# Performance work log

Hardware: AMD Instinct MI355X
Metric: run time of the kernel (lower is better)

The kernel has to match this reference:

```python
import jax, jax.numpy as jnp
import numpy as np

NEG_INF = -1e9  # matches the TF additive-mask constant


def setup_inputs() -> dict:
    key = jax.random.key(0)
    k1, k2, k3 = jax.random.split(key, 3)
    B, Tq, Tk, D = 8, 2048, 2048, 1024
    decoder_outputs = jax.random.normal(k1, (B, Tq, D), dtype=jnp.float32)
    encoder_outputs = jax.random.normal(k2, (B, Tk, D), dtype=jnp.float32)
    encoder_mask = jax.random.randint(k3, (B, Tk), 0, 2, dtype=jnp.int32)
    return {
        "decoder_outputs": decoder_outputs,
        "encoder_outputs": encoder_outputs,
        "encoder_mask": encoder_mask,
    }


def reference(decoder_outputs, encoder_outputs, encoder_mask):
    # score[b, q, k] = <dec[b, q], enc[b, k]>  (no 1/sqrt(d) scaling in original)
    score = jnp.einsum("bqd,bkd->bqk", decoder_outputs, encoder_outputs)
    m = encoder_mask.astype(score.dtype)[:, None, :]  # [B, 1, Tk]
    score = score + (1.0 - m) * NEG_INF
    attention_weights = jax.nn.softmax(score, axis=-1)
    context_vector = jnp.einsum("bqk,bkd->bqd", attention_weights, encoder_outputs)
    return (context_vector, attention_weights)
```

## Files before the change

### kernel.cpp

```cpp
#include <hip/hip_runtime.h>
#include <cstddef>
#include <cstdint>

typedef _Float16 f16x8 __attribute__((ext_vector_type(8)));
typedef _Float16 f16x4 __attribute__((ext_vector_type(4)));
typedef float f32x4 __attribute__((ext_vector_type(4)));

static constexpr int BATCH = 8;
static constexpr int TQ = 2048;
static constexpr int TK = 2048;
static constexpr int DIM = 1024;
static constexpr size_t CTX_ELEMS = (size_t)BATCH * TQ * DIM;
static constexpr size_t ATT_ELEMS = (size_t)BATCH * TQ * TK;

static constexpr size_t WS_DEC = 0;
static constexpr size_t WS_ENC = WS_DEC + CTX_ELEMS;
static constexpr size_t WS_ENCT = WS_ENC + CTX_ELEMS;
static constexpr size_t WS_W = WS_ENCT + CTX_ELEMS;
static constexpr size_t WS_NEEDED_BYTES = (WS_W + ATT_ELEMS) * 2;

__device__ __forceinline__ void async16(const void* g, const void* l) {
  __builtin_amdgcn_global_load_lds(
      (const __attribute__((address_space(1))) unsigned int*)g,
      (__attribute__((address_space(3))) unsigned int*)l, 16, 0, 0);
}

__device__ __forceinline__ f16x8 cvt8(float4 a, float4 b) {
  f16x8 h;
  h[0] = (_Float16)a.x; h[1] = (_Float16)a.y; h[2] = (_Float16)a.z; h[3] = (_Float16)a.w;
  h[4] = (_Float16)b.x; h[5] = (_Float16)b.y; h[6] = (_Float16)b.z; h[7] = (_Float16)b.w;
  return h;
}


__global__ __launch_bounds__(256) void convert_kernel(
    const float* __restrict__ enc, const float* __restrict__ dec,
    _Float16* __restrict__ enc16, _Float16* __restrict__ encT,
    _Float16* __restrict__ dec16) {
  __shared__ _Float16 sT[64 * 72];
  const int k0 = blockIdx.x * 64, d0 = blockIdx.y * 64, b = blockIdx.z;
  const int t = threadIdx.x;
  const int krow = t >> 2;
  const int dcol = (t & 3) * 16;

  const float* src = enc + ((size_t)b * TK + k0 + krow) * DIM + d0 + dcol;
  float4 f0 = *(const float4*)(src);
  float4 f1 = *(const float4*)(src + 4);
  float4 f2 = *(const float4*)(src + 8);
  float4 f3 = *(const float4*)(src + 12);
  _Float16 h[16];
#pragma unroll
  for (int i = 0; i < 4; i++) {
    h[i]      = (_Float16)((&f0.x)[i]);
    h[i + 4]  = (_Float16)((&f1.x)[i]);
    h[i + 8]  = (_Float16)((&f2.x)[i]);
    h[i + 12] = (_Float16)((&f3.x)[i]);
  }
  _Float16* dsts = enc16 + ((size_t)b * TK + k0 + krow) * DIM + d0 + dcol;
  *(f16x8*)dsts = *(const f16x8*)&h[0];
  *(f16x8*)(dsts + 8) = *(const f16x8*)&h[8];
#pragma unroll
  for (int i = 0; i < 16; i++)
    sT[(dcol + i) * 72 + krow] = h[i];

  {
    const int bid = ((blockIdx.z * gridDim.y) + blockIdx.y) * gridDim.x + blockIdx.x;
    size_t base = (size_t)bid * 4096 + (size_t)t * 16;
    float4 a0 = *(const float4*)(dec + base);
    float4 a1 = *(const float4*)(dec + base + 4);
    float4 a2 = *(const float4*)(dec + base + 8);
    float4 a3 = *(const float4*)(dec + base + 12);
    *(f16x8*)(dec16 + base) = cvt8(a0, a1);
    *(f16x8*)(dec16 + base + 8) = cvt8(a2, a3);
  }

  __syncthreads();

  const int drow = t >> 2;
  const int kg = (t & 3) * 16;
  f16x8 v0 = *(const f16x8*)&sT[drow * 72 + kg];
  f16x8 v1 = *(const f16x8*)&sT[drow * 72 + kg + 8];
  _Float16* dst = encT + ((size_t)b * DIM + d0 + drow) * TK + k0 + kg;
  *(f16x8*)dst = v0;
  *(f16x8*)(dst + 8) = v1;
}

static constexpr int HT = 8192;

template <int KD>
__device__ __forceinline__ void stage_ht(const _Float16* __restrict__ Xb,
                                         _Float16* ht, int khalf, int w, int lane) {
#pragma unroll
  for (int j = 0; j < 2; ++j) {
    const int r = w * 16 + j * 8 + (lane >> 3);
    const int slot = (lane & 7) ^ (r & 7);
    async16(Xb + (size_t)r * KD + khalf + slot * 8, ht + (w * 16 + j * 8) * 64);
  }
}

template <int M, int N, int K>
__global__ __launch_bounds__(512, 2) void gemm_cf(
    const _Float16* __restrict__ A, const _Float16* __restrict__ B,
    float* __restrict__ C) {
  __shared__ _Float16 lds[65536];
  constexpr int T = K / 64;

  const int b = blockIdx.x, nt = blockIdx.y, mt = blockIdx.z;
  const int tid = threadIdx.x;
  const int lane = tid & 63, w = tid >> 6;
  const int tm = lane & 15, quad = lane >> 4;
  const int wr = w >> 2, wc = w & 3;

  const _Float16* Ab = A + ((size_t)b * M + mt * 256) * K;
  const _Float16* Bb = B + ((size_t)b * N + nt * 256) * K;
  const _Float16* src[4] = {Ab, Ab + (size_t)128 * K, Bb, Bb + (size_t)128 * K};

  const int aht = wr;
  const int bht = 2 + (wc >> 1);
  const int brow = (wc & 1) * 64;

  const int s0 = (quad ^ (tm & 7)) * 8;
  const int s1 = s0 ^ 32;

  f32x4 acc[8][4] = {};

#pragma unroll
  for (int q = 0; q < 4; ++q)
    stage_ht<K>(src[q], lds + q * HT, 0, w, lane);
  asm volatile("s_waitcnt vmcnt(0)" ::: "memory");
  __builtin_amdgcn_s_barrier();

  for (int t = 0; t < T; ++t) {
    const int p = t & 1, np = p ^ 1;
    const _Float16* hA = lds + (p * 4 + aht) * HT;
    const _Float16* hB = lds + (p * 4 + bht) * HT;
    f16x8 aF[4], bF[4];

#pragma unroll
    for (int j = 0; j < 4; ++j)
      bF[j] = *(const f16x8*)(hB + (brow + j * 16 + tm) * 64 + s0);
#pragma unroll
    for (int i = 0; i < 4; ++i)
      aF[i] = *(const f16x8*)(hA + (i * 16 + tm) * 64 + s0);
    if (t + 1 < T) {
      const int kh = (t + 1) * 64;
#pragma unroll
      for (int q = 0; q < 4; ++q)
        stage_ht<K>(src[q], lds + (np * 4 + q) * HT, kh, w, lane);
    }
    __builtin_amdgcn_s_barrier();
    __builtin_amdgcn_s_setprio(1);
#pragma unroll
    for (int i = 0; i < 4; ++i)
#pragma unroll
      for (int j = 0; j < 4; ++j)
        acc[i][j] = __builtin_amdgcn_mfma_f32_16x16x32_f16(aF[i], bF[j], acc[i][j], 0, 0, 0);
    __builtin_amdgcn_s_setprio(0);
    __builtin_amdgcn_s_barrier();

#pragma unroll
    for (int i = 0; i < 4; ++i)
      aF[i] = *(const f16x8*)(hA + (64 + i * 16 + tm) * 64 + s0);
    __builtin_amdgcn_s_barrier();
    __builtin_amdgcn_s_setprio(1);
#pragma unroll
    for (int i = 0; i < 4; ++i)
#pragma unroll
      for (int j = 0; j < 4; ++j)
        acc[4 + i][j] = __builtin_amdgcn_mfma_f32_16x16x32_f16(aF[i], bF[j], acc[4 + i][j], 0, 0, 0);
    __builtin_amdgcn_s_setprio(0);
    __builtin_amdgcn_s_barrier();

#pragma unroll
    for (int j = 0; j < 4; ++j)
      bF[j] = *(const f16x8*)(hB + (brow + j * 16 + tm) * 64 + s1);
#pragma unroll
    for (int i = 0; i < 4; ++i)
      aF[i] = *(const f16x8*)(hA + (i * 16 + tm) * 64 + s1);
    __builtin_amdgcn_s_barrier();
    __builtin_amdgcn_s_setprio(1);
#pragma unroll
    for (int i = 0; i < 4; ++i)
#pragma unroll
      for (int j = 0; j < 4; ++j)
        acc[i][j] = __builtin_amdgcn_mfma_f32_16x16x32_f16(aF[i], bF[j], acc[i][j], 0, 0, 0);
    __builtin_amdgcn_s_setprio(0);
    __builtin_amdgcn_s_barrier();

#pragma unroll
    for (int i = 0; i < 4; ++i)
      aF[i] = *(const f16x8*)(hA + (64 + i * 16 + tm) * 64 + s1);
    __builtin_amdgcn_s_barrier();
    __builtin_amdgcn_s_setprio(1);
#pragma unroll
    for (int i = 0; i < 4; ++i)
#pragma unroll
      for (int j = 0; j < 4; ++j)
        acc[4 + i][j] = __builtin_amdgcn_mfma_f32_16x16x32_f16(aF[i], bF[j], acc[4 + i][j], 0, 0, 0);
    __builtin_amdgcn_s_setprio(0);
    asm volatile("s_waitcnt vmcnt(0)" ::: "memory");
    __builtin_amdgcn_s_barrier();
  }

#pragma unroll
  for (int i = 0; i < 8; ++i) {
#pragma unroll
    for (int rr = 0; rr < 4; ++rr) {
      size_t row = (size_t)b * M + mt * 256 + wr * 128 + i * 16 + quad * 4 + rr;
      float* Crow = C + row * (size_t)N + nt * 256 + wc * 64 + tm;
#pragma unroll
      for (int j = 0; j < 4; ++j) Crow[j * 16] = acc[i][j][rr];
    }
  }
}

__global__ __launch_bounds__(256) void softmax_kernel(
    float* __restrict__ S, const int* __restrict__ mask, _Float16* __restrict__ W16) {
  const int row = blockIdx.x;
  const int b = row >> 11;
  float* srow = S + (size_t)row * TK;
  const int* mrow = mask + (size_t)b * TK;
  const int t = threadIdx.x;

  float4 s0 = *(const float4*)(srow + t * 8);
  float4 s1 = *(const float4*)(srow + t * 8 + 4);
  int4 m0 = *(const int4*)(mrow + t * 8);
  int4 m1 = *(const int4*)(mrow + t * 8 + 4);

  float v[8] = {s0.x, s0.y, s0.z, s0.w, s1.x, s1.y, s1.z, s1.w};
  const int mm[8] = {m0.x, m0.y, m0.z, m0.w, m1.x, m1.y, m1.z, m1.w};
#pragma unroll
  for (int i = 0; i < 8; i++)
    if (!mm[i]) v[i] += -1e9f;

  float mx = v[0];
#pragma unroll
  for (int i = 1; i < 8; i++) mx = fmaxf(mx, v[i]);
#pragma unroll
  for (int off = 32; off > 0; off >>= 1) mx = fmaxf(mx, __shfl_down(mx, off));

  __shared__ float redm[4];
  __shared__ float reds[4];
  if ((t & 63) == 0) redm[t >> 6] = mx;
  __syncthreads();
  mx = fmaxf(fmaxf(redm[0], redm[1]), fmaxf(redm[2], redm[3]));

  float e[8];
  float lsum = 0.f;
#pragma unroll
  for (int i = 0; i < 8; i++) {
    e[i] = __expf(v[i] - mx);
    lsum += e[i];
  }
#pragma unroll
  for (int off = 32; off > 0; off >>= 1) lsum += __shfl_down(lsum, off);
  if ((t & 63) == 0) reds[t >> 6] = lsum;
  __syncthreads();
  const float inv = 1.0f / (reds[0] + reds[1] + reds[2] + reds[3]);

  float4 o0 = {e[0] * inv, e[1] * inv, e[2] * inv, e[3] * inv};
  float4 o1 = {e[4] * inv, e[5] * inv, e[6] * inv, e[7] * inv};
  *(float4*)(srow + t * 8) = o0;
  *(float4*)(srow + t * 8 + 4) = o1;
  if (W16) {
    f16x8 h;
    h[0] = (_Float16)o0.x; h[1] = (_Float16)o0.y; h[2] = (_Float16)o0.z; h[3] = (_Float16)o0.w;
    h[4] = (_Float16)o1.x; h[5] = (_Float16)o1.y; h[6] = (_Float16)o1.z; h[7] = (_Float16)o1.w;
    *(f16x8*)(W16 + (size_t)row * TK + t * 8) = h;
  }
}

static constexpr int BM = 128, BN = 128, BK = 32;
static constexpr int LDSS = 40;

__global__ __launch_bounds__(256) void score_kernel_fb(
    const float* __restrict__ dec, const float* __restrict__ enc,
    float* __restrict__ S) {
  __shared__ _Float16 sA[BM * LDSS];
  __shared__ _Float16 sB[BN * LDSS];
  const int nt = blockIdx.x, mt = blockIdx.y, b = blockIdx.z;
  const int t = threadIdx.x;
  const int lane = t & 63, wave = t >> 6;
  const int wm = wave >> 1, wn = wave & 1;
  const int tm = lane & 15, quad = lane >> 4;
  const float* Abase = dec + ((size_t)b * TQ + mt * BM) * DIM;
  const float* Bbase = enc + ((size_t)b * TK + nt * BN) * DIM;
  f32x4 acc[4][4] = {};
  const int r = t >> 2;
  const int c8 = (t & 3) * 8;
  for (int k0 = 0; k0 < DIM; k0 += BK) {
    float4 a0 = *(const float4*)(Abase + (size_t)r * DIM + k0 + c8);
    float4 a1 = *(const float4*)(Abase + (size_t)r * DIM + k0 + c8 + 4);
    float4 a2 = *(const float4*)(Abase + (size_t)(r + 64) * DIM + k0 + c8);
    float4 a3 = *(const float4*)(Abase + (size_t)(r + 64) * DIM + k0 + c8 + 4);
    float4 b0 = *(const float4*)(Bbase + (size_t)r * DIM + k0 + c8);
    float4 b1 = *(const float4*)(Bbase + (size_t)r * DIM + k0 + c8 + 4);
    float4 b2 = *(const float4*)(Bbase + (size_t)(r + 64) * DIM + k0 + c8);
    float4 b3 = *(const float4*)(Bbase + (size_t)(r + 64) * DIM + k0 + c8 + 4);
    __syncthreads();
    *(f16x8*)&sA[r * LDSS + c8] = cvt8(a0, a1);
    *(f16x8*)&sA[(r + 64) * LDSS + c8] = cvt8(a2, a3);
    *(f16x8*)&sB[r * LDSS + c8] = cvt8(b0, b1);
    *(f16x8*)&sB[(r + 64) * LDSS + c8] = cvt8(b2, b3);
    __syncthreads();
    f16x8 aF[4], bF[4];
#pragma unroll
    for (int i = 0; i < 4; i++)
      aF[i] = *(const f16x8*)&sA[(wm * 64 + i * 16 + tm) * LDSS + quad * 8];
#pragma unroll
    for (int j = 0; j < 4; j++)
      bF[j] = *(const f16x8*)&sB[(wn * 64 + j * 16 + tm) * LDSS + quad * 8];
#pragma unroll
    for (int i = 0; i < 4; i++)
#pragma unroll
      for (int j = 0; j < 4; j++)
        acc[i][j] = __builtin_amdgcn_mfma_f32_16x16x32_f16(aF[i], bF[j], acc[i][j], 0, 0, 0);
  }
#pragma unroll
  for (int i = 0; i < 4; i++) {
#pragma unroll
    for (int rr = 0; rr < 4; rr++) {
      size_t rowoff = ((size_t)b * TQ + mt * BM + wm * 64 + i * 16 + quad * 4 + rr) * (size_t)TK;
#pragma unroll
      for (int j = 0; j < 4; j++)
        S[rowoff + nt * BN + wn * 64 + j * 16 + tm] = acc[i][j][rr];
    }
  }
}

__global__ __launch_bounds__(256) void ctx_kernel_fb(
    const float* __restrict__ W, const float* __restrict__ enc,
    float* __restrict__ C) {
  __shared__ _Float16 sA[BM * LDSS];
  __shared__ _Float16 sB[BN * LDSS];
  const int nt = blockIdx.x;
  const int mt = blockIdx.y;
  const int b = blockIdx.z;
  const int t = threadIdx.x;
  const int lane = t & 63, wave = t >> 6;
  const int wm = wave >> 1, wn = wave & 1;
  const int tm = lane & 15, quad = lane >> 4;
  const float* Abase = W + ((size_t)b * TQ + mt * BM) * TK;
  const float* Ebase = enc + (size_t)b * TK * DIM + nt * BN;
  f32x4 acc[4][4] = {};
  const int r = t >> 2;
  const int c8 = (t & 3) * 8;
  const int kkB = (t & 7) * 4;
  const int nnB = (t >> 3) * 4;
  for (int k0 = 0; k0 < TK; k0 += BK) {
    float4 a0 = *(const float4*)(Abase + (size_t)r * TK + k0 + c8);
    float4 a1 = *(const float4*)(Abase + (size_t)r * TK + k0 + c8 + 4);
    float4 a2 = *(const float4*)(Abase + (size_t)(r + 64) * TK + k0 + c8);
    float4 a3 = *(const float4*)(Abase + (size_t)(r + 64) * TK + k0 + c8 + 4);
    float4 f[4];
#pragma unroll
    for (int i = 0; i < 4; i++)
      f[i] = *(const float4*)(Ebase + (size_t)(k0 + kkB + i) * DIM + nnB);
    __syncthreads();
    *(f16x8*)&sA[r * LDSS + c8] = cvt8(a0, a1);
    *(f16x8*)&sA[(r + 64) * LDSS + c8] = cvt8(a2, a3);
#pragma unroll
    for (int c = 0; c < 4; c++) {
      f16x4 h;
      h[0] = (_Float16)((&f[0].x)[c]);
      h[1] = (_Float16)((&f[1].x)[c]);
      h[2] = (_Float16)((&f[2].x)[c]);
      h[3] = (_Float16)((&f[3].x)[c]);
      *(f16x4*)&sB[(nnB + c) * LDSS + kkB] = h;
    }
    __syncthreads();
    f16x8 aF[4], bF[4];
#pragma unroll
    for (int i = 0; i < 4; i++)
      aF[i] = *(const f16x8*)&sA[(wm * 64 + i * 16 + tm) * LDSS + quad * 8];
#pragma unroll
    for (int j = 0; j < 4; j++)
      bF[j] = *(const f16x8*)&sB[(wn * 64 + j * 16 + tm) * LDSS + quad * 8];
#pragma unroll
    for (int i = 0; i < 4; i++)
#pragma unroll
      for (int j = 0; j < 4; j++)
        acc[i][j] = __builtin_amdgcn_mfma_f32_16x16x32_f16(aF[i], bF[j], acc[i][j], 0, 0, 0);
  }
#pragma unroll
  for (int i = 0; i < 4; i++) {
#pragma unroll
    for (int rr = 0; rr < 4; rr++) {
      size_t rowoff = ((size_t)b * TQ + mt * BM + wm * 64 + i * 16 + quad * 4 + rr) * (size_t)DIM;
#pragma unroll
      for (int j = 0; j < 4; j++)
        C[rowoff + nt * BN + wn * 64 + j * 16 + tm] = acc[i][j][rr];
    }
  }
}

extern "C" void kernel_launch(void* const* d_in, const int* in_sizes, int n_in,
                              void* d_out, int out_size, void* d_ws, size_t ws_size,
                              hipStream_t stream) {
  const float* dec = (const float*)d_in[0];
  const float* enc = (const float*)d_in[1];
  const int* mask = (const int*)d_in[2];

  float* ctx = (float*)d_out;
  float* attn = (float*)d_out + CTX_ELEMS;

  dim3 block(256);

  if (ws_size >= WS_NEEDED_BYTES) {
    _Float16* dec16 = (_Float16*)d_ws + WS_DEC;
    _Float16* enc16 = (_Float16*)d_ws + WS_ENC;
    _Float16* encT = (_Float16*)d_ws + WS_ENCT;
    _Float16* W16 = (_Float16*)d_ws + WS_W;

    convert_kernel<<<dim3(TK / 64, DIM / 64, BATCH), block, 0, stream>>>(
        enc, dec, enc16, encT, dec16);
    gemm_cf<TQ, TK, DIM><<<dim3(BATCH, TK / 256, TQ / 256), dim3(512), 0, stream>>>(dec16, enc16, attn);
    softmax_kernel<<<dim3(BATCH * TQ), block, 0, stream>>>(attn, mask, W16);
    gemm_cf<TQ, DIM, TK><<<dim3(BATCH, DIM / 256, TQ / 256), dim3(512), 0, stream>>>(W16, encT, ctx);
  } else {
    score_kernel_fb<<<dim3(TK / BN, TQ / BM, BATCH), block, 0, stream>>>(dec, enc, attn);
    softmax_kernel<<<dim3(BATCH * TQ), block, 0, stream>>>(attn, mask, nullptr);
    ctx_kernel_fb<<<dim3(DIM / BN, TQ / BM, BATCH), block, 0, stream>>>(attn, enc, ctx);
  }
}
```

Baseline: 489.1 us.

## Replace double-buffered 256x256 GEMM with triple-buffered 256x128 ring pipeline

Swaps the 256x256-tile double-buffered GEMM for a 256x128-tile kernel with a three-slot LDS ring that prefetches two k-steps ahead, using partial vmcnt waits. The 8 waves become a 4x2 grid, each holding a 64x64 accumulator instead of 128x64. This cuts per-wave register use and doubles the grid size. In exchange, the A operand is reloaded twice as often across blocks and each step does less MFMA work per barrier. The launch bounds drop the 2-blocks-per-CU hint, and the 144KB LDS footprint likely limits residency to one block per CU.

```diff
diff --git a/kernel.cpp b/kernel.cpp
--- a/kernel.cpp
+++ b/kernel.cpp
@@ -85,69 +85,69 @@
   *(f16x8*)(dst + 8) = v1;
 }
 
-static constexpr int HT = 8192;
-
-template <int KD>
-__device__ __forceinline__ void stage_ht(const _Float16* __restrict__ Xb,
-                                         _Float16* ht, int khalf, int w, int lane) {
-#pragma unroll
-  for (int j = 0; j < 2; ++j) {
-    const int r = w * 16 + j * 8 + (lane >> 3);
-    const int slot = (lane & 7) ^ (r & 7);
-    async16(Xb + (size_t)r * KD + khalf + slot * 8, ht + (w * 16 + j * 8) * 64);
-  }
-}
+static constexpr int RSLOT = 24576;
 
 template <int M, int N, int K>
-__global__ __launch_bounds__(512, 2) void gemm_cf(
+__global__ __launch_bounds__(512) void gemm_ring(
     const _Float16* __restrict__ A, const _Float16* __restrict__ B,
     float* __restrict__ C) {
-  __shared__ _Float16 lds[65536];
+  __shared__ _Float16 lds[3 * RSLOT];
   constexpr int T = K / 64;
 
   const int b = blockIdx.x, nt = blockIdx.y, mt = blockIdx.z;
   const int tid = threadIdx.x;
   const int lane = tid & 63, w = tid >> 6;
   const int tm = lane & 15, quad = lane >> 4;
-  const int wr = w >> 2, wc = w & 3;
+  const int wr = w >> 1, wc = w & 1;
 
   const _Float16* Ab = A + ((size_t)b * M + mt * 256) * K;
-  const _Float16* Bb = B + ((size_t)b * N + nt * 256) * K;
-  const _Float16* src[4] = {Ab, Ab + (size_t)128 * K, Bb, Bb + (size_t)128 * K};
-
-  const int aht = wr;
-  const int bht = 2 + (wc >> 1);
-  const int brow = (wc & 1) * 64;
+  const _Float16* Bb = B + ((size_t)b * N + nt * 128) * K;
+
+  const int srow8 = w * 8 + (lane >> 3);
+  const int schunk = (lane & 7) ^ (lane >> 3);
 
   const int s0 = (quad ^ (tm & 7)) * 8;
   const int s1 = s0 ^ 32;
 
-  f32x4 acc[8][4] = {};
-
-#pragma unroll
-  for (int q = 0; q < 4; ++q)
-    stage_ht<K>(src[q], lds + q * HT, 0, w, lane);
-  asm volatile("s_waitcnt vmcnt(0)" ::: "memory");
-  __builtin_amdgcn_s_barrier();
-
+  f32x4 acc[4][4] = {};
+
+#define STAGE_A(base, kh, j) \
+  async16(Ab + (size_t)((j)*64 + srow8) * K + (kh) + schunk * 8, \
+          (base) + ((j)*64 + w * 8) * 64)
+#define STAGE_B(base, kh, j) \
+  async16(Bb + (size_t)((j)*64 + srow8) * K + (kh) + schunk * 8, \
+          (base) + 16384 + ((j)*64 + w * 8) * 64)
+
+  {
+    _Float16* sl0 = lds;
+    _Float16* sl1 = lds + RSLOT;
+#pragma unroll
+    for (int j = 0; j < 4; ++j) STAGE_A(sl0, 0, j);
+    STAGE_B(sl0, 0, 0); STAGE_B(sl0, 0, 1);
+#pragma unroll
+    for (int j = 0; j < 4; ++j) STAGE_A(sl1, 64, j);
+    STAGE_B(sl1, 64, 0); STAGE_B(sl1, 64, 1);
+    asm volatile("s_waitcnt vmcnt(6)" ::: "memory");
+    __builtin_amdgcn_s_barrier();
+  }
+
+  int sc = 0;
   for (int t = 0; t < T; ++t) {
-    const int p = t & 1, np = p ^ 1;
-    const _Float16* hA = lds + (p * 4 + aht) * HT;
-    const _Float16* hB = lds + (p * 4 + bht) * HT;
+    const _Float16* bufA = lds + sc * RSLOT;
+    const _Float16* bufB = bufA + 16384;
+    int ss = sc + 2; if (ss >= 3) ss -= 3;
+    _Float16* st = lds + ss * RSLOT;
+    const bool pre = (t + 2 < T);
+    const int kh = (t + 2) * 64;
     f16x8 aF[4], bF[4];
 
 #pragma unroll
+    for (int i = 0; i < 4; ++i)
+      aF[i] = *(const f16x8*)(bufA + (wr * 64 + i * 16 + tm) * 64 + s0);
+#pragma unroll
     for (int j = 0; j < 4; ++j)
-      bF[j] = *(const f16x8*)(hB + (brow + j * 16 + tm) * 64 + s0);
-#pragma unroll
-    for (int i = 0; i < 4; ++i)
-      aF[i] = *(const f16x8*)(hA + (i * 16 + tm) * 64 + s0);
-    if (t + 1 < T) {
-      const int kh = (t + 1) * 64;
-#pragma unroll
-      for (int q = 0; q < 4; ++q)
-        stage_ht<K>(src[q], lds + (np * 4 + q) * HT, kh, w, lane);
-    }
+      bF[j] = *(const f16x8*)(bufB + (wc * 64 + j * 16 + tm) * 64 + s0);
+    if (pre) { STAGE_A(st, kh, 0); STAGE_A(st, kh, 1); STAGE_A(st, kh, 2); }
     __builtin_amdgcn_s_barrier();
     __builtin_amdgcn_s_setprio(1);
 #pragma unroll
@@ -160,23 +160,11 @@
 
 #pragma unroll
     for (int i = 0; i < 4; ++i)
-      aF[i] = *(const f16x8*)(hA + (64 + i * 16 + tm) * 64 + s0);
-    __builtin_amdgcn_s_barrier();
-    __builtin_amdgcn_s_setprio(1);
-#pragma unroll
-    for (int i = 0; i < 4; ++i)
-#pragma unroll
-      for (int j = 0; j < 4; ++j)
-        acc[4 + i][j] = __builtin_amdgcn_mfma_f32_16x16x32_f16(aF[i], bF[j], acc[4 + i][j], 0, 0, 0);
-    __builtin_amdgcn_s_setprio(0);
-    __builtin_amdgcn_s_barrier();
-
+      aF[i] = *(const f16x8*)(bufA + (wr * 64 + i * 16 + tm) * 64 + s1);
 #pragma unroll
     for (int j = 0; j < 4; ++j)
-      bF[j] = *(const f16x8*)(hB + (brow + j * 16 + tm) * 64 + s1);
-#pragma unroll
-    for (int i = 0; i < 4; ++i)
-      aF[i] = *(const f16x8*)(hA + (i * 16 + tm) * 64 + s1);
+      bF[j] = *(const f16x8*)(bufB + (wc * 64 + j * 16 + tm) * 64 + s1);
+    if (pre) { STAGE_A(st, kh, 3); STAGE_B(st, kh, 0); STAGE_B(st, kh, 1); }
     __builtin_amdgcn_s_barrier();
     __builtin_amdgcn_s_setprio(1);
 #pragma unroll
@@ -185,29 +173,23 @@
       for (int j = 0; j < 4; ++j)
         acc[i][j] = __builtin_amdgcn_mfma_f32_16x16x32_f16(aF[i], bF[j], acc[i][j], 0, 0, 0);
     __builtin_amdgcn_s_setprio(0);
+    if (pre) {
+      asm volatile("s_waitcnt vmcnt(6)" ::: "memory");
+    } else if (t + 2 == T) {
+      asm volatile("s_waitcnt vmcnt(0)" ::: "memory");
+    }
     __builtin_amdgcn_s_barrier();
-
-#pragma unroll
-    for (int i = 0; i < 4; ++i)
-      aF[i] = *(const f16x8*)(hA + (64 + i * 16 + tm) * 64 + s1);
-    __builtin_amdgcn_s_barrier();
-    __builtin_amdgcn_s_setprio(1);
-#pragma unroll
-    for (int i = 0; i < 4; ++i)
-#pragma unroll
-      for (int j = 0; j < 4; ++j)
-        acc[4 + i][j] = __builtin_amdgcn_mfma_f32_16x16x32_f16(aF[i], bF[j], acc[4 + i][j], 0, 0, 0);
-    __builtin_amdgcn_s_setprio(0);
-    asm volatile("s_waitcnt vmcnt(0)" ::: "memory");
-    __builtin_amdgcn_s_barrier();
-  }
-
-#pragma unroll
-  for (int i = 0; i < 8; ++i) {
+    sc += 1; if (sc >= 3) sc = 0;
+  }
+#undef STAGE_A
+#undef STAGE_B
+
+#pragma unroll
+  for (int i = 0; i < 4; ++i) {
 #pragma unroll
     for (int rr = 0; rr < 4; ++rr) {
-      size_t row = (size_t)b * M + mt * 256 + wr * 128 + i * 16 + quad * 4 + rr;
-      float* Crow = C + row * (size_t)N + nt * 256 + wc * 64 + tm;
+      size_t row = (size_t)b * M + mt * 256 + wr * 64 + i * 16 + quad * 4 + rr;
+      float* Crow = C + row * (size_t)N + nt * 128 + wc * 64 + tm;
 #pragma unroll
       for (int j = 0; j < 4; ++j) Crow[j * 16] = acc[i][j][rr];
     }
@@ -414,9 +396,9 @@
 
     convert_kernel<<<dim3(TK / 64, DIM / 64, BATCH), block, 0, stream>>>(
         enc, dec, enc16, encT, dec16);
-    gemm_cf<TQ, TK, DIM><<<dim3(BATCH, TK / 256, TQ / 256), dim3(512), 0, stream>>>(dec16, enc16, attn);
+    gemm_ring<TQ, TK, DIM><<<dim3(BATCH, TK / 128, TQ / 256), dim3(512), 0, stream>>>(dec16, enc16, attn);
     softmax_kernel<<<dim3(BATCH * TQ), block, 0, stream>>>(attn, mask, W16);
-    gemm_cf<TQ, DIM, TK><<<dim3(BATCH, DIM / 256, TQ / 256), dim3(512), 0, stream>>>(W16, encT, ctx);
+    gemm_ring<TQ, DIM, TK><<<dim3(BATCH, DIM / 128, TQ / 256), dim3(512), 0, stream>>>(W16, encT, ctx);
   } else {
     score_kernel_fb<<<dim3(TK / BN, TQ / BM, BATCH), block, 0, stream>>>(dec, enc, attn);
     softmax_kernel<<<dim3(BATCH * TQ), block, 0, stream>>>(attn, mask, nullptr);
```

Result: slower. 506.9 us (+3.6%).
